# Optimization experiments

Measured on AMD Instinct MI355X. Metric: run time of the kernel, lower is better.

The kernel has to match this reference:

```python
import jax, jax.numpy as jnp
import numpy as np

N, K, E = 50000, 16, 200000
HID, NL, H = 128, 3, 4
NT, NCV = 8, 17          # node types; categorical vocab = 16 values + 1 unknown
D = HID // H             # head dim = 32


def setup_inputs() -> dict:
    key = jax.random.key(0)
    ks = jax.random.split(key, 20)

    def rn(i, shape, scale=0.05):
        return jax.random.normal(ks[i], shape, dtype=jnp.float32) * scale

    return {
        # graph structure / attributes (int constants)
        "type_idx": jax.random.randint(ks[0], (N,), 0, NT),
        "cat_idx": jax.random.randint(ks[1], (N, 2), 0, NCV),
        "nbr_idx": jax.random.randint(ks[2], (N, K), 0, N),
        "nbr_mask": jax.random.randint(ks[3], (N, K), 0, 2).astype(bool),
        "edges": jax.random.randint(ks[4], (E, 2), 0, N),
        # float node/edge features
        "log_deg": jax.random.uniform(ks[5], (N, 1), dtype=jnp.float32) * 5.0,  # log(deg+1)
        "edge_feats": jax.random.uniform(ks[6], (E, 2), dtype=jnp.float32) * 2.0,  # [temporal, hop]
        # parameters
        "type_embed": rn(7, (NT, HID // 2)),
        "cat_embed0": rn(8, (NCV, HID // 4)),
        "cat_embed1": rn(9, (NCV, HID // 4)),
        "deg_W": rn(10, (1, HID // 4), 0.1),
        "deg_b": jnp.zeros((HID // 4,), jnp.float32),
        "proj_W": rn(11, (HID // 2 + 2 * (HID // 4) + HID // 4, HID)),  # 160 -> 128
        "proj_b": jnp.zeros((HID,), jnp.float32),
        "attn_Wqkv": rn(12, (NL, HID, 3 * HID)),
        "attn_bqkv": jnp.zeros((NL, 3 * HID), jnp.float32),
        "attn_Wo": rn(13, (NL, HID, HID)),
        "attn_bo": jnp.zeros((NL, HID), jnp.float32),
        "eW1": rn(14, (2 * HID + 2, HID)),
        "eb1": jnp.zeros((HID,), jnp.float32),
        "eW2": rn(15, (HID, HID // 2)),
        "eb2": jnp.zeros((HID // 2,), jnp.float32),
        "eW3": rn(16, (HID // 2, 1)),
        "eb3": jnp.zeros((1,), jnp.float32),
    }


def reference(type_idx, cat_idx, nbr_idx, nbr_mask, edges, log_deg, edge_feats,
              type_embed, cat_embed0, cat_embed1, deg_W, deg_b, proj_W, proj_b,
              attn_Wqkv, attn_bqkv, attn_Wo, attn_bo,
              eW1, eb1, eW2, eb2, eW3, eb3):
    n = type_idx.shape[0]
    # --- encode_node_features ---
    feats = jnp.concatenate([
        type_embed[type_idx],                       # [N, 64]
        cat_embed0[cat_idx[:, 0]],                  # [N, 32]
        cat_embed1[cat_idx[:, 1]],                  # [N, 32]
        jax.nn.relu(log_deg @ deg_W + deg_b),       # [N, 32]
    ], axis=-1)
    x = feats @ proj_W + proj_b                     # [N, HID]

    # context = [self] + neighbors, exactly as the per-node loop builds it
    ctx_idx = jnp.concatenate([jnp.arange(n)[:, None], nbr_idx], axis=1)   # [N, K+1]
    ctx_mask = jnp.concatenate([jnp.ones((n, 1), bool), nbr_mask], axis=1)  # [N, K+1]
    has_nbr = nbr_mask.any(axis=1)                  # nodes w/o neighbors skip attention
    C = ctx_idx.shape[1]
    scale = 1.0 / jnp.sqrt(jnp.float32(D))

    # --- encode_nodes: per-layer single-query MHA over local context ---
    for l in range(NL):
        qkv = x @ attn_Wqkv[l] + attn_bqkv[l]       # [N, 3*HID]
        q, k, v = jnp.split(qkv, 3, axis=-1)
        qh = q.reshape(n, H, D)                     # [N, H, D]
        kh = k[ctx_idx].reshape(n, C, H, D)         # neighbor gather
        vh = v[ctx_idx].reshape(n, C, H, D)
        scores = jnp.einsum('nhd,nchd->nhc', qh, kh) * scale   # [N, H, C]
        scores = jnp.where(ctx_mask[:, None, :], scores, -1e9)
        attn = jax.nn.softmax(scores, axis=-1)
        o = jnp.einsum('nhc,nchd->nhd', attn, vh).reshape(n, HID)
        o = o @ attn_Wo[l] + attn_bo[l]
        x = jax.nn.relu(jnp.where(has_nbr[:, None], o, x))

    # --- edge scoring MLP (dropout inactive at inference) ---
    h = jnp.concatenate([x[edges[:, 0]], x[edges[:, 1]], edge_feats], axis=-1)  # [E, 258]
    h = jax.nn.relu(h @ eW1 + eb1)
    h = jax.nn.relu(h @ eW2 + eb2)
    return (h @ eW3 + eb3)[:, 0]                    # [E] logits
```

## Files before the change

kernel.cpp:

```cpp
#include <hip/hip_runtime.h>
#include <math.h>

#define HID 128

typedef _Float16 f16x8 __attribute__((ext_vector_type(8)));
typedef float    f32x4 __attribute__((ext_vector_type(4)));

static __device__ __forceinline__ float h_lo(unsigned p) {
    return (float)__builtin_bit_cast(_Float16, (unsigned short)p);
}
static __device__ __forceinline__ float h_hi(unsigned p) {
    return (float)__builtin_bit_cast(_Float16, (unsigned short)(p >> 16));
}
static __device__ __forceinline__ unsigned pack2h(float x, float y) {
    const unsigned short lx = __builtin_bit_cast(unsigned short, (_Float16)x);
    const unsigned short ly = __builtin_bit_cast(unsigned short, (_Float16)y);
    return ((unsigned)ly << 16) | lx;
}

__global__ __launch_bounds__(256) void prep_kernel(
    const float* __restrict__ Wqkv, const float* __restrict__ Wo,
    const float* __restrict__ W1, const float* __restrict__ W2,
    const float* __restrict__ Wproj,
    _Float16* __restrict__ dst)
{
    const int idx = blockIdx.x * 256 + threadIdx.x;
    if (idx < 147456) {
        const int l = idx / 49152, t = idx % 49152;
        const int j = t & 7, ln = (t >> 3) & 63, kk = (t >> 9) & 3, nt = t >> 11;
        const int k = kk * 32 + (ln >> 4) * 8 + j, n = nt * 16 + (ln & 15);
        dst[idx] = (_Float16)Wqkv[((size_t)l * 128 + k) * 384 + n];
    } else if (idx < 196608) {
        const int t0 = idx - 147456;
        const int l = t0 / 16384, t = t0 % 16384;
        const int j = t & 7, ln = (t >> 3) & 63, kk = (t >> 9) & 3, nt = t >> 11;
        const int k = kk * 32 + (ln >> 4) * 8 + j, n = nt * 16 + (ln & 15);
        dst[idx] = (_Float16)Wo[((size_t)l * 128 + k) * 128 + n];
    } else if (idx < 229376) {
        const int t = idx - 196608;
        const int j = t & 7, ln = (t >> 3) & 63, kk = (t >> 9) & 7, nt = t >> 12;
        const int k = kk * 32 + (ln >> 4) * 8 + j, n = nt * 16 + (ln & 15);
        dst[idx] = (_Float16)W1[k * 128 + n];
    } else if (idx < 237568) {
        const int t = idx - 229376;
        const int j = t & 7, ln = (t >> 3) & 63, kk = (t >> 9) & 3, nt = t >> 11;
        const int k = kk * 32 + (ln >> 4) * 8 + j, n = nt * 16 + (ln & 15);
        dst[idx] = (_Float16)W2[k * 64 + n];
    } else if (idx < 258048) {
        const int t = idx - 237568;
        const int j = t & 7, ln = (t >> 3) & 63;
        const int blk = t >> 9;
        const int kk = blk % 5, nt = blk / 5;
        const int k = kk * 32 + (ln >> 4) * 8 + j, n = nt * 16 + (ln & 15);
        dst[idx] = (_Float16)Wproj[k * 128 + n];
    }
}

#define TILE_STORE(dst)                                                        \
    _Pragma("unroll")                                                          \
    for (int t = 0; t < 4; ++t) {                                              \
        const int lr  = t * 4 + (lane >> 4);                                   \
        const int j16 = lane & 15;                                             \
        const f16x8 v = *(const f16x8*)(tb + lr * 256 + ((j16 * 16) ^ (lr << 4))); \
        if (base + lr < n)                                                     \
            *(f16x8*)((dst) + (size_t)(base + lr) * 128 + j16 * 8) = v;        \
    }

#define QKV_PHASE(A2, WQ, BQKV)                                                \
    {                                                                          \
        _Float16* outs[3] = {qh, kh, vh};                                      \
        _Pragma("unroll")                                                      \
        for (int part = 0; part < 3; ++part) {                                 \
            f32x4 C[8];                                                        \
            _Pragma("unroll")                                                  \
            for (int nt = 0; nt < 8; ++nt) C[nt] = (f32x4){0.f, 0.f, 0.f, 0.f};\
            _Pragma("unroll")                                                  \
            for (int kk = 0; kk < 4; ++kk) {                                   \
                _Pragma("unroll")                                              \
                for (int nt = 0; nt < 8; ++nt) {                               \
                    const f16x8 bf = *(const f16x8*)((WQ) + (((part * 8 + nt) * 4 + kk) << 9) + lane * 8); \
                    C[nt] = __builtin_amdgcn_mfma_f32_16x16x32_f16((A2)[kk], bf, C[nt], 0, 0, 0); \
                }                                                              \
            }                                                                  \
            _Pragma("unroll")                                                  \
            for (int nt = 0; nt < 8; ++nt) {                                   \
                const int nn = nt * 16 + c;                                    \
                const float bb = (BQKV)[part * 128 + nn];                      \
                _Pragma("unroll")                                              \
                for (int r = 0; r < 4; ++r) {                                  \
                    const int rr = g * 4 + r;                                  \
                    *(_Float16*)(tb + rr * 256 + ((nn * 2) ^ (rr << 4))) = (_Float16)(C[nt][r] + bb); \
                }                                                              \
            }                                                                  \
            _Float16* const dst = outs[part];                                  \
            TILE_STORE(dst)                                                    \
        }                                                                      \
    }

__global__ __launch_bounds__(256) void encode_qkv_kernel(
    const int* __restrict__ type_idx, const int* __restrict__ cat_idx,
    const float* __restrict__ log_deg,
    const float* __restrict__ type_embed, const float* __restrict__ cat0,
    const float* __restrict__ cat1, const float* __restrict__ deg_W,
    const float* __restrict__ deg_b,
    const _Float16* __restrict__ wprojp, const float* __restrict__ proj_b,
    const _Float16* __restrict__ wq, const float* __restrict__ bqkv,
    _Float16* __restrict__ xh,
    _Float16* __restrict__ qh, _Float16* __restrict__ kh, _Float16* __restrict__ vh,
    int n)
{
    __shared__ __align__(16) _Float16 tile[4][16 * 128];
    const int wave = threadIdx.x >> 6;
    const int lane = threadIdx.x & 63;
    const int g = lane >> 4, c = lane & 15;
    const int base = (blockIdx.x * 4 + wave) * 16;
    if (base >= n) return;
    const int arow = min(base + c, n - 1);
    char* const tb = (char*)&tile[wave][0];

    const int  ti = type_idx[arow];
    const int  c0 = cat_idx[arow * 2 + 0];
    const int  c1 = cat_idx[arow * 2 + 1];
    const float ld = log_deg[arow];
    f16x8 a[5];
    {
        const float* srcs[4] = {
            type_embed + ti * 64 + g * 8,
            type_embed + ti * 64 + 32 + g * 8,
            cat0 + c0 * 32 + g * 8,
            cat1 + c1 * 32 + g * 8,
        };
        #pragma unroll
        for (int kk = 0; kk < 4; ++kk) {
            const float4 v0 = *(const float4*)(srcs[kk]);
            const float4 v1 = *(const float4*)(srcs[kk] + 4);
            a[kk] = (f16x8){(_Float16)v0.x, (_Float16)v0.y, (_Float16)v0.z, (_Float16)v0.w,
                            (_Float16)v1.x, (_Float16)v1.y, (_Float16)v1.z, (_Float16)v1.w};
        }
        const float4 w0 = *(const float4*)(deg_W + g * 8);
        const float4 w1 = *(const float4*)(deg_W + g * 8 + 4);
        const float4 d0 = *(const float4*)(deg_b + g * 8);
        const float4 d1 = *(const float4*)(deg_b + g * 8 + 4);
        a[4] = (f16x8){
            (_Float16)fmaxf(ld * w0.x + d0.x, 0.f), (_Float16)fmaxf(ld * w0.y + d0.y, 0.f),
            (_Float16)fmaxf(ld * w0.z + d0.z, 0.f), (_Float16)fmaxf(ld * w0.w + d0.w, 0.f),
            (_Float16)fmaxf(ld * w1.x + d1.x, 0.f), (_Float16)fmaxf(ld * w1.y + d1.y, 0.f),
            (_Float16)fmaxf(ld * w1.z + d1.z, 0.f), (_Float16)fmaxf(ld * w1.w + d1.w, 0.f)};
    }

    f32x4 Cp[8];
    #pragma unroll
    for (int nt = 0; nt < 8; ++nt) Cp[nt] = (f32x4){0.f, 0.f, 0.f, 0.f};
    #pragma unroll
    for (int kk = 0; kk < 5; ++kk) {
        #pragma unroll
        for (int nt = 0; nt < 8; ++nt) {
            const f16x8 bf = *(const f16x8*)(wprojp + ((nt * 5 + kk) << 9) + lane * 8);
            Cp[nt] = __builtin_amdgcn_mfma_f32_16x16x32_f16(a[kk], bf, Cp[nt], 0, 0, 0);
        }
    }
    #pragma unroll
    for (int nt = 0; nt < 8; ++nt) {
        const int nn = nt * 16 + c;
        const float bb = proj_b[nn];
        #pragma unroll
        for (int r = 0; r < 4; ++r) {
            const int rr = g * 4 + r;
            *(_Float16*)(tb + rr * 256 + ((nn * 2) ^ (rr << 4))) = (_Float16)(Cp[nt][r] + bb);
        }
    }
    TILE_STORE(xh)

    f16x8 a2[4];
    #pragma unroll
    for (int kk = 0; kk < 4; ++kk)
        a2[kk] = *(const f16x8*)(tb + c * 256 + ((kk * 64 + g * 16) ^ (c << 4)));
    QKV_PHASE(a2, wq, bqkv)
}

__global__ __launch_bounds__(256) void projqkv_kernel(
    const _Float16* __restrict__ oh, const int* __restrict__ mask,
    const _Float16* __restrict__ xh_prev,
    const _Float16* __restrict__ wo, const float* __restrict__ bo,
    const _Float16* __restrict__ wq, const float* __restrict__ bqkv,
    _Float16* __restrict__ xh_next,
    _Float16* __restrict__ qh, _Float16* __restrict__ kh, _Float16* __restrict__ vh,
    int do_qkv, int n)
{
    __shared__ __align__(16) _Float16 tile[4][16 * 128];
    const int wave = threadIdx.x >> 6;
    const int lane = threadIdx.x & 63;
    const int g = lane >> 4, c = lane & 15;
    const int base = (blockIdx.x * 4 + wave) * 16;
    if (base >= n) return;
    const int arow = min(base + c, n - 1);
    char* const tb = (char*)&tile[wave][0];

    f32x4 Cp[8];
    #pragma unroll
    for (int nt = 0; nt < 8; ++nt) Cp[nt] = (f32x4){0.f, 0.f, 0.f, 0.f};
    #pragma unroll
    for (int kk = 0; kk < 4; ++kk) {
        const f16x8 a = *(const f16x8*)(oh + (size_t)arow * 128 + kk * 32 + g * 8);
        #pragma unroll
        for (int nt = 0; nt < 8; ++nt) {
            const f16x8 bf = *(const f16x8*)(wo + ((nt * 4 + kk) << 9) + lane * 8);
            Cp[nt] = __builtin_amdgcn_mfma_f32_16x16x32_f16(a, bf, Cp[nt], 0, 0, 0);
        }
    }
    int mk[4]; int rrow[4];
    #pragma unroll
    for (int r = 0; r < 4; ++r) {
        rrow[r] = min(base + g * 4 + r, n - 1);
        mk[r] = mask[rrow[r]];
    }
    #pragma unroll
    for (int nt = 0; nt < 8; ++nt) {
        const int nn = nt * 16 + c;
        const float bb = bo[nn];
        #pragma unroll
        for (int r = 0; r < 4; ++r) {
            float val = Cp[nt][r] + bb;
            if (!mk[r]) val = (float)xh_prev[(size_t)rrow[r] * 128 + nn];
            val = fmaxf(val, 0.0f);
            const int rr = g * 4 + r;
            *(_Float16*)(tb + rr * 256 + ((nn * 2) ^ (rr << 4))) = (_Float16)val;
        }
    }
    TILE_STORE(xh_next)
    if (!do_qkv) return;

    f16x8 a2[4];
    #pragma unroll
    for (int kk = 0; kk < 4; ++kk)
        a2[kk] = *(const f16x8*)(tb + c * 256 + ((kk * 64 + g * 16) ^ (c << 4)));
    QKV_PHASE(a2, wq, bqkv)
}

__global__ __launch_bounds__(256) void attn_kernel(
    const _Float16* __restrict__ qh, const _Float16* __restrict__ kh,
    const _Float16* __restrict__ vh,
    const int* __restrict__ nbr_idx, const int* __restrict__ nbr_mask,
    _Float16* __restrict__ oh, int* __restrict__ mask_out, int n)
{
    const int wave = threadIdx.x >> 6;
    const int lane = threadIdx.x & 63;
    const float scale = 0.17677669529663687f;
    const int base = (blockIdx.x * 4 + wave) * 4;
    if (base >= n) return;
    const int nbc = min(4, n - base);
    for (int nb = 0; nb < nbc; ++nb) {
        const int node = base + nb;
        const unsigned qq = *(const unsigned*)(qh + (size_t)node * HID + lane * 2);
        const float qx = h_lo(qq), qy = h_hi(qq);
        float s[17];
        int cix[17];
        int anyn = 0;
        #pragma unroll
        for (int c = 0; c < 17; ++c) {
            int cidx, valid;
            if (c == 0) { cidx = node; valid = 1; }
            else {
                cidx  = nbr_idx[node * 16 + (c - 1)];
                valid = nbr_mask[node * 16 + (c - 1)];
                anyn |= valid;
            }
            cix[c] = cidx;
            const unsigned kk = *(const unsigned*)(kh + (size_t)cidx * HID + lane * 2);
            float p = qx * h_lo(kk) + qy * h_hi(kk);
            p += __shfl_xor(p, 1);
            p += __shfl_xor(p, 2);
            p += __shfl_xor(p, 4);
            p += __shfl_xor(p, 8);
            s[c] = valid ? p * scale : -1e9f;
        }
        if (lane == 0) mask_out[node] = anyn;
        float mx = s[0];
        #pragma unroll
        for (int c = 1; c < 17; ++c) mx = fmaxf(mx, s[c]);
        float sum = 0.0f;
        #pragma unroll
        for (int c = 0; c < 17; ++c) { s[c] = __expf(s[c] - mx); sum += s[c]; }
        const float inv = 1.0f / sum;
        float ox = 0.0f, oy = 0.0f;
        #pragma unroll
        for (int c = 0; c < 17; ++c) {
            const unsigned vv = *(const unsigned*)(vh + (size_t)cix[c] * HID + lane * 2);
            const float a = s[c] * inv;
            ox += a * h_lo(vv);
            oy += a * h_hi(vv);
        }
        *(unsigned*)(oh + (size_t)node * HID + lane * 2) = pack2h(ox, oy);
    }
}

__global__ __launch_bounds__(256) void edge_mfma_kernel(
    const _Float16* __restrict__ xh,
    const int* __restrict__ edges,
    const float* __restrict__ edge_feats,
    const _Float16* __restrict__ w1p,
    const _Float16* __restrict__ w2p,
    const float* __restrict__ W1,
    const float* __restrict__ b1,
    const float* __restrict__ b2,
    const float* __restrict__ W3, const float* __restrict__ b3,
    float* __restrict__ out, int ne)
{
    __shared__ __align__(16) _Float16 h1s[4][16 * 128];
    const int wave = threadIdx.x >> 6;
    const int lane = threadIdx.x & 63;
    const int g = lane >> 4, c = lane & 15;
    const int base = (blockIdx.x * 4 + wave) * 16;
    if (base >= ne) return;

    const int erow = min(base + c, ne - 1);
    const int e0 = edges[erow * 2 + 0];
    const int e1 = edges[erow * 2 + 1];

    f32x4 C1[8];
    #pragma unroll
    for (int nt = 0; nt < 8; ++nt) C1[nt] = (f32x4){0.f, 0.f, 0.f, 0.f};
    #pragma unroll
    for (int kk = 0; kk < 8; ++kk) {
        const int node = (kk < 4) ? e0 : e1;
        const f16x8 a = *(const f16x8*)(xh + (size_t)node * 128 + (kk & 3) * 32 + g * 8);
        #pragma unroll
        for (int nt = 0; nt < 8; ++nt) {
            const f16x8 bf = *(const f16x8*)(w1p + ((nt * 8 + kk) << 9) + lane * 8);
            C1[nt] = __builtin_amdgcn_mfma_f32_16x16x32_f16(a, bf, C1[nt], 0, 0, 0);
        }
    }

    float ef0[4], ef1[4];
    #pragma unroll
    for (int r = 0; r < 4; ++r) {
        const int m = min(base + g * 4 + r, ne - 1);
        ef0[r] = edge_feats[(size_t)m * 2 + 0];
        ef1[r] = edge_feats[(size_t)m * 2 + 1];
    }
    char* const h1base = (char*)&h1s[wave][0];
    #pragma unroll
    for (int nt = 0; nt < 8; ++nt) {
        const int nn  = nt * 16 + c;
        const float bb  = b1[nn];
        const float wc0 = W1[256 * 128 + nn];
        const float wc1 = W1[257 * 128 + nn];
        #pragma unroll
        for (int r = 0; r < 4; ++r) {
            const int rr = g * 4 + r;
            const float h = fmaxf(C1[nt][r] + bb + ef0[r] * wc0 + ef1[r] * wc1, 0.0f);
            *(_Float16*)(h1base + rr * 256 + ((nn * 2) ^ (rr << 4))) = (_Float16)h;
        }
    }

    f32x4 C2[4];
    #pragma unroll
    for (int nt = 0; nt < 4; ++nt) C2[nt] = (f32x4){0.f, 0.f, 0.f, 0.f};
    #pragma unroll
    for (int kk = 0; kk < 4; ++kk) {
        const int k0b = kk * 64 + g * 16;
        const f16x8 a = *(const f16x8*)(h1base + c * 256 + (k0b ^ (c << 4)));
        #pragma unroll
        for (int nt = 0; nt < 4; ++nt) {
            const f16x8 bf = *(const f16x8*)(w2p + ((nt * 4 + kk) << 9) + lane * 8);
            C2[nt] = __builtin_amdgcn_mfma_f32_16x16x32_f16(a, bf, C2[nt], 0, 0, 0);
        }
    }

    const float bb3 = b3[0];
    #pragma unroll
    for (int r = 0; r < 4; ++r) {
        float acc = 0.0f;
        #pragma unroll
        for (int nt = 0; nt < 4; ++nt) {
            const int n2 = nt * 16 + c;
            acc += fmaxf(C2[nt][r] + b2[n2], 0.0f) * W3[n2];
        }
        acc += __shfl_xor(acc, 1);
        acc += __shfl_xor(acc, 2);
        acc += __shfl_xor(acc, 4);
        acc += __shfl_xor(acc, 8);
        const int m = base + g * 4 + r;
        if (c == 0 && m < ne) out[m] = acc + bb3;
    }
}

extern "C" void kernel_launch(void* const* d_in, const int* in_sizes, int n_in,
                              void* d_out, int out_size, void* d_ws, size_t ws_size,
                              hipStream_t stream) {
    const int*   type_idx   = (const int*)d_in[0];
    const int*   cat_idx    = (const int*)d_in[1];
    const int*   nbr_idx    = (const int*)d_in[2];
    const int*   nbr_mask   = (const int*)d_in[3];
    const int*   edges      = (const int*)d_in[4];
    const float* log_deg    = (const float*)d_in[5];
    const float* edge_feats = (const float*)d_in[6];
    const float* type_embed = (const float*)d_in[7];
    const float* cat0       = (const float*)d_in[8];
    const float* cat1       = (const float*)d_in[9];
    const float* deg_W      = (const float*)d_in[10];
    const float* deg_b      = (const float*)d_in[11];
    const float* proj_W     = (const float*)d_in[12];
    const float* proj_b     = (const float*)d_in[13];
    const float* attn_Wqkv  = (const float*)d_in[14];
    const float* attn_bqkv  = (const float*)d_in[15];
    const float* attn_Wo    = (const float*)d_in[16];
    const float* attn_bo    = (const float*)d_in[17];
    const float* eW1        = (const float*)d_in[18];
    const float* eb1        = (const float*)d_in[19];
    const float* eW2        = (const float*)d_in[20];
    const float* eb2        = (const float*)d_in[21];
    const float* eW3        = (const float*)d_in[22];
    const float* eb3        = (const float*)d_in[23];

    const int n  = in_sizes[0];
    const int ne = in_sizes[4] / 2;
    float* out = (float*)d_out;

    _Float16* xhA = (_Float16*)d_ws;
    _Float16* xhB = xhA + (size_t)n * HID;
    _Float16* qh  = xhB + (size_t)n * HID;
    _Float16* kh  = qh  + (size_t)n * HID;
    _Float16* vh  = kh  + (size_t)n * HID;
    _Float16* oh  = vh  + (size_t)n * HID;
    _Float16* wpk = oh  + (size_t)n * HID;
    int* mask = (int*)(wpk + 258048);
    _Float16* wqkvp[3] = {wpk, wpk + 49152, wpk + 98304};
    _Float16* wop[3]   = {wpk + 147456, wpk + 163840, wpk + 180224};
    _Float16* w1p    = wpk + 196608;
    _Float16* w2p    = wpk + 229376;
    _Float16* wprojp = wpk + 237568;

    prep_kernel<<<dim3(1008), dim3(256), 0, stream>>>(
        attn_Wqkv, attn_Wo, eW1, eW2, proj_W, wpk);

    const int gemm_grid = (n + 63) / 64;
    const int attn_grid = (n + 15) / 16;

    encode_qkv_kernel<<<dim3(gemm_grid), dim3(256), 0, stream>>>(
        type_idx, cat_idx, log_deg, type_embed, cat0, cat1, deg_W, deg_b,
        wprojp, proj_b, wqkvp[0], attn_bqkv,
        xhA, qh, kh, vh, n);
    attn_kernel<<<dim3(attn_grid), dim3(256), 0, stream>>>(
        qh, kh, vh, nbr_idx, nbr_mask, oh, mask, n);

    projqkv_kernel<<<dim3(gemm_grid), dim3(256), 0, stream>>>(
        oh, mask, xhA, wop[0], attn_bo, wqkvp[1], attn_bqkv + 384,
        xhB, qh, kh, vh, 1, n);
    attn_kernel<<<dim3(attn_grid), dim3(256), 0, stream>>>(
        qh, kh, vh, nbr_idx, nbr_mask, oh, mask, n);

    projqkv_kernel<<<dim3(gemm_grid), dim3(256), 0, stream>>>(
        oh, mask, xhB, wop[1], attn_bo + 128, wqkvp[2], attn_bqkv + 768,
        xhA, qh, kh, vh, 1, n);
    attn_kernel<<<dim3(attn_grid), dim3(256), 0, stream>>>(
        qh, kh, vh, nbr_idx, nbr_mask, oh, mask, n);

    projqkv_kernel<<<dim3(gemm_grid), dim3(256), 0, stream>>>(
        oh, mask, xhA, wop[2], attn_bo + 256, nullptr, nullptr,
        xhB, nullptr, nullptr, nullptr, 0, n);

    const int edge_grid = (ne + 63) / 64;
    edge_mfma_kernel<<<dim3(edge_grid), dim3(256), 0, stream>>>(
        xhB, edges, edge_feats, w1p, w2p, eW1, eb1, eb2, eW3, eb3, out, ne);
}
```

Baseline: 459.4 us.

## Interleave K and V rows and prefetch both before attention scoring

Measured after the change: 445.0 us. -3.1%, faster.

```diff
diff --git a/kernel.cpp b/kernel.cpp
--- a/kernel.cpp
+++ b/kernel.cpp
@@ -56,19 +56,18 @@
     }
 }
 
-#define TILE_STORE(dst)                                                        \
+#define TILE_STORE_S(dst, rowstride)                                           \
     _Pragma("unroll")                                                          \
     for (int t = 0; t < 4; ++t) {                                              \
         const int lr  = t * 4 + (lane >> 4);                                   \
         const int j16 = lane & 15;                                             \
         const f16x8 v = *(const f16x8*)(tb + lr * 256 + ((j16 * 16) ^ (lr << 4))); \
         if (base + lr < n)                                                     \
-            *(f16x8*)((dst) + (size_t)(base + lr) * 128 + j16 * 8) = v;        \
+            *(f16x8*)((dst) + (size_t)(base + lr) * (rowstride) + j16 * 8) = v;\
     }
 
 #define QKV_PHASE(A2, WQ, BQKV)                                                \
     {                                                                          \
-        _Float16* outs[3] = {qh, kh, vh};                                      \
         _Pragma("unroll")                                                      \
         for (int part = 0; part < 3; ++part) {                                 \
             f32x4 C[8];                                                        \
@@ -92,8 +91,9 @@
                     *(_Float16*)(tb + rr * 256 + ((nn * 2) ^ (rr << 4))) = (_Float16)(C[nt][r] + bb); \
                 }                                                              \
             }                                                                  \
-            _Float16* const dst = outs[part];                                  \
-            TILE_STORE(dst)                                                    \
+            if (part == 0)      { TILE_STORE_S(qh, 128) }                      \
+            else if (part == 1) { TILE_STORE_S(kvh, 256) }                     \
+            else                { TILE_STORE_S(kvh + 128, 256) }               \
         }                                                                      \
     }
 
@@ -106,7 +106,7 @@
     const _Float16* __restrict__ wprojp, const float* __restrict__ proj_b,
     const _Float16* __restrict__ wq, const float* __restrict__ bqkv,
     _Float16* __restrict__ xh,
-    _Float16* __restrict__ qh, _Float16* __restrict__ kh, _Float16* __restrict__ vh,
+    _Float16* __restrict__ qh, _Float16* __restrict__ kvh,
     int n)
 {
     __shared__ __align__(16) _Float16 tile[4][16 * 128];
@@ -169,7 +169,7 @@
             *(_Float16*)(tb + rr * 256 + ((nn * 2) ^ (rr << 4))) = (_Float16)(Cp[nt][r] + bb);
         }
     }
-    TILE_STORE(xh)
+    TILE_STORE_S(xh, 128)
 
     f16x8 a2[4];
     #pragma unroll
@@ -184,7 +184,7 @@
     const _Float16* __restrict__ wo, const float* __restrict__ bo,
     const _Float16* __restrict__ wq, const float* __restrict__ bqkv,
     _Float16* __restrict__ xh_next,
-    _Float16* __restrict__ qh, _Float16* __restrict__ kh, _Float16* __restrict__ vh,
+    _Float16* __restrict__ qh, _Float16* __restrict__ kvh,
     int do_qkv, int n)
 {
     __shared__ __align__(16) _Float16 tile[4][16 * 128];
@@ -227,7 +227,7 @@
             *(_Float16*)(tb + rr * 256 + ((nn * 2) ^ (rr << 4))) = (_Float16)val;
         }
     }
-    TILE_STORE(xh_next)
+    TILE_STORE_S(xh_next, 128)
     if (!do_qkv) return;
 
     f16x8 a2[4];
@@ -238,43 +238,47 @@
 }
 
 __global__ __launch_bounds__(256) void attn_kernel(
-    const _Float16* __restrict__ qh, const _Float16* __restrict__ kh,
-    const _Float16* __restrict__ vh,
+    const _Float16* __restrict__ qh, const _Float16* __restrict__ kvh,
     const int* __restrict__ nbr_idx, const int* __restrict__ nbr_mask,
     _Float16* __restrict__ oh, int* __restrict__ mask_out, int n)
 {
     const int wave = threadIdx.x >> 6;
     const int lane = threadIdx.x & 63;
     const float scale = 0.17677669529663687f;
-    const int base = (blockIdx.x * 4 + wave) * 4;
+    const int base = (blockIdx.x * 4 + wave) * 2;
     if (base >= n) return;
-    const int nbc = min(4, n - base);
+    const int nbc = min(2, n - base);
     for (int nb = 0; nb < nbc; ++nb) {
         const int node = base + nb;
         const unsigned qq = *(const unsigned*)(qh + (size_t)node * HID + lane * 2);
         const float qx = h_lo(qq), qy = h_hi(qq);
+        int valid[17];
+        int anyn = 0;
+        unsigned kw[17], vw[17];
+        #pragma unroll
+        for (int c = 0; c < 17; ++c) {
+            int cidx;
+            if (c == 0) { cidx = node; valid[c] = 1; }
+            else {
+                cidx = nbr_idx[node * 16 + (c - 1)];
+                valid[c] = nbr_mask[node * 16 + (c - 1)];
+                anyn |= valid[c];
+            }
+            const _Float16* kv = kvh + (size_t)cidx * 256;
+            kw[c] = *(const unsigned*)(kv + lane * 2);
+            vw[c] = *(const unsigned*)(kv + 128 + lane * 2);
+        }
+        if (lane == 0) mask_out[node] = anyn;
         float s[17];
-        int cix[17];
-        int anyn = 0;
         #pragma unroll
         for (int c = 0; c < 17; ++c) {
-            int cidx, valid;
-            if (c == 0) { cidx = node; valid = 1; }
-            else {
-                cidx  = nbr_idx[node * 16 + (c - 1)];
-                valid = nbr_mask[node * 16 + (c - 1)];
-                anyn |= valid;
-            }
-            cix[c] = cidx;
-            const unsigned kk = *(const unsigned*)(kh + (size_t)cidx * HID + lane * 2);
-            float p = qx * h_lo(kk) + qy * h_hi(kk);
+            float p = qx * h_lo(kw[c]) + qy * h_hi(kw[c]);
             p += __shfl_xor(p, 1);
             p += __shfl_xor(p, 2);
             p += __shfl_xor(p, 4);
             p += __shfl_xor(p, 8);
-            s[c] = valid ? p * scale : -1e9f;
-        }
-        if (lane == 0) mask_out[node] = anyn;
+            s[c] = valid[c] ? p * scale : -1e9f;
+        }
         float mx = s[0];
         #pragma unroll
         for (int c = 1; c < 17; ++c) mx = fmaxf(mx, s[c]);
@@ -285,10 +289,9 @@
         float ox = 0.0f, oy = 0.0f;
         #pragma unroll
         for (int c = 0; c < 17; ++c) {
-            const unsigned vv = *(const unsigned*)(vh + (size_t)cix[c] * HID + lane * 2);
             const float a = s[c] * inv;
-            ox += a * h_lo(vv);
-            oy += a * h_hi(vv);
+            ox += a * h_lo(vw[c]);
+            oy += a * h_hi(vw[c]);
         }
         *(unsigned*)(oh + (size_t)node * HID + lane * 2) = pack2h(ox, oy);
     }
@@ -420,9 +423,8 @@
     _Float16* xhA = (_Float16*)d_ws;
     _Float16* xhB = xhA + (size_t)n * HID;
     _Float16* qh  = xhB + (size_t)n * HID;
-    _Float16* kh  = qh  + (size_t)n * HID;
-    _Float16* vh  = kh  + (size_t)n * HID;
-    _Float16* oh  = vh  + (size_t)n * HID;
+    _Float16* kvh = qh  + (size_t)n * HID;
+    _Float16* oh  = kvh + (size_t)n * 256;
     _Float16* wpk = oh  + (size_t)n * HID;
     int* mask = (int*)(wpk + 258048);
     _Float16* wqkvp[3] = {wpk, wpk + 49152, wpk + 98304};
@@ -435,30 +437,30 @@
         attn_Wqkv, attn_Wo, eW1, eW2, proj_W, wpk);
 
     const int gemm_grid = (n + 63) / 64;
-    const int attn_grid = (n + 15) / 16;
+    const int attn_grid = (n + 7) / 8;
 
     encode_qkv_kernel<<<dim3(gemm_grid), dim3(256), 0, stream>>>(
         type_idx, cat_idx, log_deg, type_embed, cat0, cat1, deg_W, deg_b,
         wprojp, proj_b, wqkvp[0], attn_bqkv,
-        xhA, qh, kh, vh, n);
+        xhA, qh, kvh, n);
     attn_kernel<<<dim3(attn_grid), dim3(256), 0, stream>>>(
-        qh, kh, vh, nbr_idx, nbr_mask, oh, mask, n);
+        qh, kvh, nbr_idx, nbr_mask, oh, mask, n);
 
     projqkv_kernel<<<dim3(gemm_grid), dim3(256), 0, stream>>>(
         oh, mask, xhA, wop[0], attn_bo, wqkvp[1], attn_bqkv + 384,
-        xhB, qh, kh, vh, 1, n);
+        xhB, qh, kvh, 1, n);
     attn_kernel<<<dim3(attn_grid), dim3(256), 0, stream>>>(
-        qh, kh, vh, nbr_idx, nbr_mask, oh, mask, n);
+        qh, kvh, nbr_idx, nbr_mask, oh, mask, n);
 
     projqkv_kernel<<<dim3(gemm_grid), dim3(256), 0, stream>>>(
         oh, mask, xhB, wop[1], attn_bo + 128, wqkvp[2], attn_bqkv + 768,
-        xhA, qh, kh, vh, 1, n);
+        xhA, qh, kvh, 1, n);
     attn_kernel<<<dim3(attn_grid), dim3(256), 0, stream>>>(
-        qh, kh, vh, nbr_idx, nbr_mask, oh, mask, n);
+        qh, kvh, nbr_idx, nbr_mask, oh, mask, n);
 
     projqkv_kernel<<<dim3(gemm_grid), dim3(256), 0, stream>>>(
         oh, mask, xhA, wop[2], attn_bo + 256, nullptr, nullptr,
-        xhB, nullptr, nullptr, nullptr, 0, n);
+        xhB, nullptr, nullptr, 0, n);
 
     const int edge_grid = (ne + 63) / 64;
     edge_mfma_kernel<<<dim3(edge_grid), dim3(256), 0, stream>>>(
```
